# Performance work log

Hardware: AMD Instinct MI355X
Metric: run time of the kernel (lower is better)

Reference implementation:

```python
import jax, jax.numpy as jnp
import numpy as np

N = 4096       # num nodes
E = 131072     # num edges (avg degree 32)
IN = 128       # in_channels
H = 256        # hidden_channels
NC = 16        # num_classes
NH = 4         # num_heads
HD = H // NH   # head dim
EPS = 1e-5


def setup_inputs() -> dict:
    key = jax.random.key(0)
    ks = jax.random.split(key, 16)
    p = lambda k, sh, s=0.05: jax.random.normal(k, sh, jnp.float32) * s
    return {
        "x": jax.random.normal(ks[0], (N, IN), jnp.float32),
        "edge_index": jax.random.randint(ks[1], (2, E), 0, N),
        "edge_attr": jax.random.uniform(ks[2], (E,), jnp.float32),
        # GCN layers
        "W_gcn1": p(ks[3], (IN, H)), "b_gcn1": jnp.zeros((H,), jnp.float32),
        "W_gcn2": p(ks[4], (H, H)), "b_gcn2": jnp.zeros((H,), jnp.float32),
        # Transformer encoder layer (post-norm, batch_first)
        "in_proj_w": p(ks[5], (3 * H, H)), "in_proj_b": jnp.zeros((3 * H,), jnp.float32),
        "out_proj_w": p(ks[6], (H, H)), "out_proj_b": jnp.zeros((H,), jnp.float32),
        "ln1_g": jnp.ones((H,), jnp.float32), "ln1_b": jnp.zeros((H,), jnp.float32),
        "ffn_w1": p(ks[7], (H, 4 * H)), "ffn_b1": jnp.zeros((4 * H,), jnp.float32),
        "ffn_w2": p(ks[8], (4 * H, H)), "ffn_b2": jnp.zeros((H,), jnp.float32),
        "ln2_g": jnp.ones((H,), jnp.float32), "ln2_b": jnp.zeros((H,), jnp.float32),
        # classifier head
        "W_cls": p(ks[9], (H, NC)), "b_cls": jnp.zeros((NC,), jnp.float32),
        # semantic decoder
        "W_d1": p(ks[10], (H, 2 * H)), "b_d1": jnp.zeros((2 * H,), jnp.float32),
        "W_d2": p(ks[11], (2 * H, 3)), "b_d2": jnp.zeros((3,), jnp.float32),
    }


def gcn_conv(x, edge_index, edge_weight, W, b):
    """PyG GCNConv: add self-loops, symmetric norm, gather-matmul-scatter."""
    n = x.shape[0]
    src, dst = edge_index[0], edge_index[1]
    loop = jnp.arange(n)
    src_f = jnp.concatenate([src, loop])
    dst_f = jnp.concatenate([dst, loop])
    ew_f = jnp.concatenate([edge_weight, jnp.ones((n,), x.dtype)])
    deg = jax.ops.segment_sum(ew_f, dst_f, num_segments=n)
    dinv = jnp.where(deg > 0, jax.lax.rsqrt(deg), 0.0)
    norm = dinv[src_f] * ew_f * dinv[dst_f]            # [E+N]
    h = x @ W                                          # [N,H]
    out = jax.ops.segment_sum(norm[:, None] * h[src_f], dst_f, num_segments=n)
    return out + b


def layer_norm(x, g, b):
    mu = jnp.mean(x, axis=-1, keepdims=True)
    var = jnp.mean(jnp.square(x - mu), axis=-1, keepdims=True)
    return (x - mu) * jax.lax.rsqrt(var + EPS) * g + b


def transformer_layer(x, in_proj_w, in_proj_b, out_proj_w, out_proj_b,
                      ln1_g, ln1_b, ffn_w1, ffn_b1, ffn_w2, ffn_b2, ln2_g, ln2_b):
    # Self-attention (seq = all N nodes, batch of 1), eval mode (no dropout)
    qkv = x @ in_proj_w.T + in_proj_b                  # [N,3H]
    q, k, v = jnp.split(qkv, 3, axis=-1)
    q = q.reshape(-1, NH, HD) * (1.0 / np.sqrt(HD))
    k = k.reshape(-1, NH, HD)
    v = v.reshape(-1, NH, HD)
    scores = jnp.einsum("nhd,mhd->hnm", q, k)          # [NH,N,N]
    attn = jax.nn.softmax(scores, axis=-1)
    ctx = jnp.einsum("hnm,mhd->nhd", attn, v).reshape(-1, H)
    attn_out = ctx @ out_proj_w.T + out_proj_b
    x = layer_norm(x + attn_out, ln1_g, ln1_b)         # post-norm
    ffn = jax.nn.relu(x @ ffn_w1 + ffn_b1) @ ffn_w2 + ffn_b2
    return layer_norm(x + ffn, ln2_g, ln2_b)


def reference(x, edge_index, edge_attr,
              W_gcn1, b_gcn1, W_gcn2, b_gcn2,
              in_proj_w, in_proj_b, out_proj_w, out_proj_b,
              ln1_g, ln1_b, ffn_w1, ffn_b1, ffn_w2, ffn_b2, ln2_g, ln2_b,
              W_cls, b_cls, W_d1, b_d1, W_d2, b_d2):
    x_local = jax.nn.relu(gcn_conv(x, edge_index, edge_attr, W_gcn1, b_gcn1))
    # F.dropout with training=False is identity
    x_local = gcn_conv(x_local, edge_index, edge_attr, W_gcn2, b_gcn2)
    x_global = transformer_layer(x_local, in_proj_w, in_proj_b, out_proj_w,
                                 out_proj_b, ln1_g, ln1_b, ffn_w1, ffn_b1,
                                 ffn_w2, ffn_b2, ln2_g, ln2_b)
    x_final = x_local + x_global
    out_cls = jax.nn.log_softmax(x_final @ W_cls + b_cls, axis=1)
    out_reco = jax.nn.sigmoid(jax.nn.relu(x_final @ W_d1 + b_d1) @ W_d2 + b_d2)
    return (out_cls, out_reco)
```

## Files before the change

### kernel.cpp

```cpp
#include <hip/hip_runtime.h>
#include <hip/hip_bf16.h>

#define N_NODES 4096
#define N_EDGES 131072
#define KSPLIT 4

typedef short bf16x8 __attribute__((ext_vector_type(8)));
typedef float f32x4  __attribute__((ext_vector_type(4)));

static __device__ __forceinline__ float b2f(__hip_bfloat16 x) { return __bfloat162float(x); }
static __device__ __forceinline__ __hip_bfloat16 f2b(float x) { return __float2bfloat16(x); }
static __device__ __forceinline__ short f2bs(float x) {
    __hip_bfloat16 h = __float2bfloat16(x);
    return *reinterpret_cast<short*>(&h);
}
static __device__ __forceinline__ float us2f(ushort u) {
    union { unsigned i; float f; } x; x.i = ((unsigned)u) << 16; return x.f;
}

static __device__ __forceinline__ float rmax16(float v) {
    v = fmaxf(v, __shfl_xor(v, 1));
    v = fmaxf(v, __shfl_xor(v, 2));
    v = fmaxf(v, __shfl_xor(v, 4));
    v = fmaxf(v, __shfl_xor(v, 8));
    return v;
}
static __device__ __forceinline__ float rsum16(float v) {
    v += __shfl_xor(v, 1);
    v += __shfl_xor(v, 2);
    v += __shfl_xor(v, 4);
    v += __shfl_xor(v, 8);
    return v;
}

__global__ void probe_k(const unsigned* __restrict__ ln1g_raw,
                        const unsigned* __restrict__ ei_raw, int* flags) {
    if (threadIdx.x == 0 && blockIdx.x == 0) {
        flags[0] = (ln1g_raw[0] == 0x3F800000u) ? 1 : 0;
        unsigned acc = 0;
        for (int j = 1; j < 32; j += 2) acc |= ei_raw[j];
        flags[1] = (acc == 0u) ? 1 : 0;
    }
}

struct Ptrs24 { const void* p[24]; };

#define CAST_TOTAL 1681171

__global__ __launch_bounds__(256) void cast_all(Ptrs24 ptrs, const int* __restrict__ flags,
                                                __hip_bfloat16* __restrict__ canon) {
    const int sizes[24] = {524288,131072,32768,256,65536,256,196608,768,65536,256,
                           256,256,262144,1024,262144,256,256,256,4096,16,
                           131072,512,1536,3};
    int i = blockIdx.x * 256 + threadIdx.x;
    if (i >= CAST_TOTAL) return;
    const int f32 = flags[0];
    int off = i, seg = 0, base = 0;
    bool done = false;
#pragma unroll
    for (int s = 0; s < 24; s++) {
        if (!done) {
            if (off < sizes[s]) { seg = s; done = true; }
            else { off -= sizes[s]; base += sizes[s]; }
        }
    }
    float v = f32 ? ((const float*)ptrs.p[seg])[off]
                  : b2f(((const __hip_bfloat16*)ptrs.p[seg])[off]);
    int dst = off;
    if (seg == 2)       dst = (off & 255)  * 128  + (off >> 8);
    else if (seg == 4)  dst = (off & 255)  * 256  + (off >> 8);
    else if (seg == 12) dst = (off & 1023) * 256  + (off >> 10);
    else if (seg == 14) dst = (off & 255)  * 1024 + (off >> 8);
    else if (seg == 20) dst = (off & 511)  * 256  + (off >> 9);
    canon[base + dst] = f2b(v);
}

static __device__ __forceinline__ int ld_idx(const void* ei, int k, int i64) {
    return i64 ? (int)((const long long*)ei)[k] : ((const int*)ei)[k];
}

__global__ __launch_bounds__(256) void deg_init_k(float* deg, int* cnt) {
    int i = blockIdx.x * 256 + threadIdx.x;
    if (i < N_NODES) { deg[i] = 1.0f; cnt[i] = 0; }
}

__global__ __launch_bounds__(256) void deg_scat_k(const void* __restrict__ ei,
                                                  const __hip_bfloat16* __restrict__ ew,
                                                  const int* __restrict__ flags,
                                                  float* deg, int* cnt) {
    int e = blockIdx.x * 256 + threadIdx.x;
    if (e < N_EDGES) {
        int d = ld_idx(ei, N_EDGES + e, flags[1]);
        atomicAdd(&deg[d], b2f(ew[e]));
        atomicAdd(&cnt[d], 1);
    }
}

__global__ __launch_bounds__(256) void scan_k(const float* __restrict__ deg, float* dinv,
                                              int* cnt, int* rowptr) {
    __shared__ int ss[256];
    const int t = threadIdx.x;
    const int base = t * 16;
    int loc[16];
    int run = 0;
#pragma unroll
    for (int j = 0; j < 16; j++) { loc[j] = run; run += cnt[base + j]; }
    ss[t] = run;
    __syncthreads();
    for (int off = 1; off < 256; off <<= 1) {
        int v = (t >= off) ? ss[t - off] : 0;
        __syncthreads();
        ss[t] += v;
        __syncthreads();
    }
    int pre = (t == 0) ? 0 : ss[t - 1];
#pragma unroll
    for (int j = 0; j < 16; j++) rowptr[base + j] = pre + loc[j];
    if (t == 255) rowptr[N_NODES] = pre + run;
    for (int i = t; i < N_NODES; i += 256) {
        float dg = deg[i];
        dinv[i] = dg > 0.f ? rsqrtf(dg) : 0.f;
        cnt[i] = 0;
    }
}

__global__ __launch_bounds__(256) void fill_k(const void* __restrict__ ei,
                                              const __hip_bfloat16* __restrict__ ew,
                                              const int* __restrict__ flags,
                                              const float* __restrict__ dinv,
                                              const int* __restrict__ rowptr,
                                              int* cur, int* csrc, float* cw) {
    int e = blockIdx.x * 256 + threadIdx.x;
    if (e < N_EDGES) {
        int i64 = flags[1];
        int s = ld_idx(ei, e, i64), d = ld_idx(ei, N_EDGES + e, i64);
        int p = atomicAdd(&cur[d], 1);
        int slot = rowptr[d] + p;
        csrc[slot] = s;
        cw[slot] = dinv[s] * b2f(ew[e]) * dinv[d];
    }
}

template <bool RELU>
__global__ __launch_bounds__(256) void gcn_agg(const __hip_bfloat16* __restrict__ hf,
                                               const float* __restrict__ dinv,
                                               const int* __restrict__ rowptr,
                                               const int* __restrict__ csrc,
                                               const float* __restrict__ cw,
                                               const __hip_bfloat16* __restrict__ bias,
                                               __hip_bfloat16* __restrict__ out) {
    const int t = threadIdx.x;
    const int n = blockIdx.x * 4 + (t >> 6);
    const int c0 = (t & 63) * 4;
    const ushort* hp = (const ushort*)hf;
    const float di = dinv[n];
    float acc[4];
    {
        ushort4 own = *(const ushort4*)(hp + (size_t)n * 256 + c0);
        ushort4 bv  = *(const ushort4*)((const ushort*)bias + c0);
        const float dii = di * di;
        acc[0] = fmaf(dii, us2f(own.x), us2f(bv.x));
        acc[1] = fmaf(dii, us2f(own.y), us2f(bv.y));
        acc[2] = fmaf(dii, us2f(own.z), us2f(bv.z));
        acc[3] = fmaf(dii, us2f(own.w), us2f(bv.w));
    }
    int p = rowptr[n];
    const int end = rowptr[n + 1];
    for (; p + 4 <= end; p += 4) {
        int s0 = csrc[p], s1 = csrc[p + 1], s2 = csrc[p + 2], s3 = csrc[p + 3];
        float w0 = cw[p], w1 = cw[p + 1], w2 = cw[p + 2], w3 = cw[p + 3];
        ushort4 v0 = *(const ushort4*)(hp + (size_t)s0 * 256 + c0);
        ushort4 v1 = *(const ushort4*)(hp + (size_t)s1 * 256 + c0);
        ushort4 v2 = *(const ushort4*)(hp + (size_t)s2 * 256 + c0);
        ushort4 v3 = *(const ushort4*)(hp + (size_t)s3 * 256 + c0);
        acc[0] = fmaf(w0, us2f(v0.x), acc[0]); acc[1] = fmaf(w0, us2f(v0.y), acc[1]);
        acc[2] = fmaf(w0, us2f(v0.z), acc[2]); acc[3] = fmaf(w0, us2f(v0.w), acc[3]);
        acc[0] = fmaf(w1, us2f(v1.x), acc[0]); acc[1] = fmaf(w1, us2f(v1.y), acc[1]);
        acc[2] = fmaf(w1, us2f(v1.z), acc[2]); acc[3] = fmaf(w1, us2f(v1.w), acc[3]);
        acc[0] = fmaf(w2, us2f(v2.x), acc[0]); acc[1] = fmaf(w2, us2f(v2.y), acc[1]);
        acc[2] = fmaf(w2, us2f(v2.z), acc[2]); acc[3] = fmaf(w2, us2f(v2.w), acc[3]);
        acc[0] = fmaf(w3, us2f(v3.x), acc[0]); acc[1] = fmaf(w3, us2f(v3.y), acc[1]);
        acc[2] = fmaf(w3, us2f(v3.z), acc[2]); acc[3] = fmaf(w3, us2f(v3.w), acc[3]);
    }
    for (; p < end; p++) {
        int s = csrc[p];
        float wgt = cw[p];
        ushort4 v = *(const ushort4*)(hp + (size_t)s * 256 + c0);
        acc[0] = fmaf(wgt, us2f(v.x), acc[0]); acc[1] = fmaf(wgt, us2f(v.y), acc[1]);
        acc[2] = fmaf(wgt, us2f(v.z), acc[2]); acc[3] = fmaf(wgt, us2f(v.w), acc[3]);
    }
    if (RELU) {
#pragma unroll
        for (int j = 0; j < 4; j++) acc[j] = fmaxf(acc[j], 0.f);
    }
    ushort4 o;
    o.x = (ushort)f2bs(acc[0]); o.y = (ushort)f2bs(acc[1]);
    o.z = (ushort)f2bs(acc[2]); o.w = (ushort)f2bs(acc[3]);
    *(ushort4*)((ushort*)out + (size_t)n * 256 + c0) = o;
}

template <bool BIAS, bool RELU>
__global__ __launch_bounds__(256) void gemm64(const __hip_bfloat16* __restrict__ A,
                                              const __hip_bfloat16* __restrict__ Bt,
                                              const __hip_bfloat16* __restrict__ bias,
                                              __hip_bfloat16* __restrict__ C,
                                              int K, int Nn) {
    __shared__ __align__(16) short As[64 * 40];
    __shared__ __align__(16) short Bs[64 * 40];
    const int t = threadIdx.x;
    const int m0 = blockIdx.y * 64, n0 = blockIdx.x * 64;
    const int lane = t & 63, w = t >> 6, li = lane & 15, g = lane >> 4;

    f32x4 acc[4];
#pragma unroll
    for (int i = 0; i < 4; i++) acc[i] = (f32x4){0.f, 0.f, 0.f, 0.f};

    const int arow = (t * 8) >> 5;
    const int acol = (t * 8) & 31;

    for (int k0 = 0; k0 < K; k0 += 32) {
        {
            uint4 v = *(const uint4*)((const ushort*)A + (size_t)(m0 + arow) * K + k0 + acol);
            *(uint4*)&As[arow * 40 + acol] = v;
            uint4 b = *(const uint4*)((const ushort*)Bt + (size_t)(n0 + arow) * K + k0 + acol);
            *(uint4*)&Bs[arow * 40 + acol] = b;
        }
        __syncthreads();
        bf16x8 a = *(const bf16x8*)&As[(w * 16 + li) * 40 + g * 8];
#pragma unroll
        for (int nt = 0; nt < 4; nt++) {
            bf16x8 b = *(const bf16x8*)&Bs[(nt * 16 + li) * 40 + g * 8];
            acc[nt] = __builtin_amdgcn_mfma_f32_16x16x32_bf16(a, b, acc[nt], 0, 0, 0);
        }
        __syncthreads();
    }
#pragma unroll
    for (int nt = 0; nt < 4; nt++) {
        const int col = n0 + nt * 16 + li;
        const float bv = BIAS ? b2f(bias[col]) : 0.f;
#pragma unroll
        for (int r = 0; r < 4; r++) {
            const int row = m0 + w * 16 + g * 4 + r;
            float v = acc[nt][r] + bv;
            if (RELU) v = fmaxf(v, 0.f);
            C[(size_t)row * Nn + col] = f2b(v);
        }
    }
}

__global__ __launch_bounds__(256) void attn_part(const __hip_bfloat16* __restrict__ qkv,
                                                 float* __restrict__ Opart,
                                                 float2* __restrict__ MLpart) {
    __shared__ __align__(16) short Qs[64 * 72];
    __shared__ __align__(16) short Ks[64 * 72];
    __shared__ __align__(16) short Vt[64 * 72];
    __shared__ __align__(16) short Ps[64 * 72];
    const int t = threadIdx.x;
    const int h = blockIdx.y;
    const int q0 = blockIdx.x * 64;
    const int kz = blockIdx.z;
    const int lane = t & 63, w = t >> 6, li = lane & 15, g = lane >> 4;

#pragma unroll
    for (int it = 0; it < 2; it++) {
        int idx = it * 256 + t;
        int r = idx >> 3, d = (idx & 7) * 8;
        uint4 v = *(const uint4*)((const ushort*)qkv + (size_t)(q0 + r) * 768 + h * 64 + d);
        *(uint4*)&Qs[r * 72 + d] = v;
    }

    f32x4 O[4];
#pragma unroll
    for (int i = 0; i < 4; i++) O[i] = (f32x4){0.f, 0.f, 0.f, 0.f};
    float m_run[4], l_run[4];
#pragma unroll
    for (int r = 0; r < 4; r++) { m_run[r] = -1e30f; l_run[r] = 0.f; }

    const int jbeg = kz * 1024;
    for (int j0 = jbeg; j0 < jbeg + 1024; j0 += 64) {
#pragma unroll
        for (int it = 0; it < 2; it++) {
            int idx = it * 256 + t;
            int r = idx >> 3, d = (idx & 7) * 8;
            uint4 kv = *(const uint4*)((const ushort*)qkv + (size_t)(j0 + r) * 768 + 256 + h * 64 + d);
            *(uint4*)&Ks[r * 72 + d] = kv;
        }
#pragma unroll
        for (int it = 0; it < 2; it++) {
            int dblk = it * 4 + w;
            uint4 vv = *(const uint4*)((const ushort*)qkv + (size_t)(j0 + lane) * 768 + 512 + h * 64 + dblk * 8);
            const short* sv = (const short*)&vv;
#pragma unroll
            for (int j = 0; j < 8; j++) Vt[(dblk * 8 + j) * 72 + lane] = sv[j];
        }
        __syncthreads();

        f32x4 S[4];
#pragma unroll
        for (int i = 0; i < 4; i++) S[i] = (f32x4){0.f, 0.f, 0.f, 0.f};
#pragma unroll
        for (int kk = 0; kk < 64; kk += 32) {
            bf16x8 a = *(const bf16x8*)&Qs[(w * 16 + li) * 72 + kk + g * 8];
#pragma unroll
            for (int nt = 0; nt < 4; nt++) {
                bf16x8 b = *(const bf16x8*)&Ks[(nt * 16 + li) * 72 + kk + g * 8];
                S[nt] = __builtin_amdgcn_mfma_f32_16x16x32_bf16(a, b, S[nt], 0, 0, 0);
            }
        }

        float alpha[4];
#pragma unroll
        for (int r = 0; r < 4; r++) {
            float mx = -1e30f;
#pragma unroll
            for (int nt = 0; nt < 4; nt++) {
                S[nt][r] *= 0.125f;
                mx = fmaxf(mx, S[nt][r]);
            }
            mx = rmax16(mx);
            float mnew = fmaxf(m_run[r], mx);
            alpha[r] = __expf(m_run[r] - mnew);
            m_run[r] = mnew;
            float rs = 0.f;
#pragma unroll
            for (int nt = 0; nt < 4; nt++) {
                float p = __expf(S[nt][r] - mnew);
                S[nt][r] = p;
                rs += p;
            }
            rs = rsum16(rs);
            l_run[r] = l_run[r] * alpha[r] + rs;
        }
#pragma unroll
        for (int nt = 0; nt < 4; nt++)
#pragma unroll
            for (int r = 0; r < 4; r++) {
                Ps[(w * 16 + g * 4 + r) * 72 + nt * 16 + li] = f2bs(S[nt][r]);
                O[nt][r] *= alpha[r];
            }
        __syncthreads();

#pragma unroll
        for (int kk = 0; kk < 64; kk += 32) {
            bf16x8 a = *(const bf16x8*)&Ps[(w * 16 + li) * 72 + kk + g * 8];
#pragma unroll
            for (int nt = 0; nt < 4; nt++) {
                bf16x8 b = *(const bf16x8*)&Vt[(nt * 16 + li) * 72 + kk + g * 8];
                O[nt] = __builtin_amdgcn_mfma_f32_16x16x32_bf16(a, b, O[nt], 0, 0, 0);
            }
        }
        __syncthreads();
    }

    const int hb = kz * 4 + h;
#pragma unroll
    for (int nt = 0; nt < 4; nt++)
#pragma unroll
        for (int r = 0; r < 4; r++) {
            int lr = w * 16 + g * 4 + r;
            Opart[((size_t)hb * 4096 + q0 + lr) * 64 + nt * 16 + li] = O[nt][r];
        }
    if (li == 0) {
#pragma unroll
        for (int r = 0; r < 4; r++) {
            int lr = w * 16 + g * 4 + r;
            MLpart[(size_t)hb * 4096 + q0 + lr] = make_float2(m_run[r], l_run[r]);
        }
    }
}

__global__ __launch_bounds__(256) void attn_comb(const float* __restrict__ Opart,
                                                 const float2* __restrict__ MLpart,
                                                 __hip_bfloat16* __restrict__ ctx) {
    const int t = threadIdx.x;
    const int h = blockIdx.y;
    const int row = blockIdx.x * 64 + (t >> 2);
    const int d0 = (t & 3) * 16;
    float m[KSPLIT], l[KSPLIT];
    float M = -1e30f;
#pragma unroll
    for (int s = 0; s < KSPLIT; s++) {
        float2 ml = MLpart[(size_t)(s * 4 + h) * 4096 + row];
        m[s] = ml.x; l[s] = ml.y;
        M = fmaxf(M, m[s]);
    }
    float L = 0.f, wgt[KSPLIT];
#pragma unroll
    for (int s = 0; s < KSPLIT; s++) { wgt[s] = __expf(m[s] - M); L += l[s] * wgt[s]; }
    const float inv = 1.f / L;
    float o[16];
#pragma unroll
    for (int j = 0; j < 16; j++) o[j] = 0.f;
#pragma unroll
    for (int s = 0; s < KSPLIT; s++) {
        const float* base = Opart + ((size_t)(s * 4 + h) * 4096 + row) * 64 + d0;
#pragma unroll
        for (int q = 0; q < 4; q++) {
            f32x4 v = *(const f32x4*)(base + q * 4);
#pragma unroll
            for (int j = 0; j < 4; j++) o[q * 4 + j] = fmaf(wgt[s], v[j], o[q * 4 + j]);
        }
    }
    ushort pk[16];
#pragma unroll
    for (int j = 0; j < 16; j++) pk[j] = (ushort)f2bs(o[j] * inv);
    ushort* dst = (ushort*)ctx + (size_t)row * 256 + h * 64 + d0;
    *(uint4*)dst = *(uint4*)pk;
    *(uint4*)(dst + 8) = *(uint4*)(pk + 8);
}

template <bool ADDC>
__global__ __launch_bounds__(256) void ln256(const __hip_bfloat16* __restrict__ A,
                                             const __hip_bfloat16* __restrict__ Bv,
                                             const __hip_bfloat16* __restrict__ gw,
                                             const __hip_bfloat16* __restrict__ bw,
                                             const __hip_bfloat16* __restrict__ Cadd,
                                             __hip_bfloat16* __restrict__ out) {
    __shared__ float red[8];
    const int row = blockIdx.x, c = threadIdx.x;
    const size_t o = (size_t)row * 256 + c;
    float x = b2f(A[o]) + b2f(Bv[o]);
    float s = x;
#pragma unroll
    for (int m = 1; m < 64; m <<= 1) s += __shfl_xor(s, m);
    const int wv = c >> 6;
    if ((c & 63) == 0) red[wv] = s;
    __syncthreads();
    float mu = (red[0] + red[1] + red[2] + red[3]) * (1.f / 256.f);
    float d = x - mu;
    float s2 = d * d;
#pragma unroll
    for (int m = 1; m < 64; m <<= 1) s2 += __shfl_xor(s2, m);
    if ((c & 63) == 0) red[4 + wv] = s2;
    __syncthreads();
    float var = (red[4] + red[5] + red[6] + red[7]) * (1.f / 256.f);
    float y = d * rsqrtf(var + 1e-5f) * b2f(gw[c]) + b2f(bw[c]);
    if (ADDC) y += b2f(Cadd[o]);
    out[o] = f2b(y);
}

__global__ __launch_bounds__(256) void cls16(const __hip_bfloat16* __restrict__ xf,
                                             const __hip_bfloat16* __restrict__ W,
                                             const __hip_bfloat16* __restrict__ b,
                                             const int* __restrict__ flags,
                                             void* __restrict__ out) {
    __shared__ float Ws[256 * 16];
    __shared__ float bs[16];
    const int t = threadIdx.x;
    for (int i = t; i < 4096; i += 256) Ws[i] = b2f(W[i]);
    if (t < 16) bs[t] = b2f(b[t]);
    __syncthreads();
    const int c = t & 15, rl = t >> 4;
    const int row = blockIdx.x * 16 + rl;
    const ushort* xr = (const ushort*)xf + (size_t)row * 256;
    float acc = bs[c];
    for (int k0 = 0; k0 < 256; k0 += 8) {
        uint4 v = *(const uint4*)(xr + k0);
        const ushort* sv = (const ushort*)&v;
#pragma unroll
        for (int j = 0; j < 8; j++) acc = fmaf(us2f(sv[j]), Ws[(k0 + j) * 16 + c], acc);
    }
    float mx = rmax16(acc);
    float se = rsum16(__expf(acc - mx));
    float v = acc - mx - __logf(se);
    const size_t oidx = (size_t)row * 16 + c;
    if (flags[0]) ((float*)out)[oidx] = v;
    else          ((__hip_bfloat16*)out)[oidx] = f2b(v);
}

__global__ __launch_bounds__(256) void reco3(const __hip_bfloat16* __restrict__ hid,
                                             const __hip_bfloat16* __restrict__ W,
                                             const __hip_bfloat16* __restrict__ b,
                                             const int* __restrict__ flags,
                                             void* __restrict__ out) {
    __shared__ float Ws[512 * 3];
    const int t = threadIdx.x;
    for (int i = t; i < 1536; i += 256) Ws[i] = b2f(W[i]);
    __syncthreads();
    const int c = t & 3, rl = t >> 2;
    const int row = blockIdx.x * 64 + rl;
    if (c < 3) {
        float acc = b2f(b[c]);
        const ushort* hr = (const ushort*)hid + (size_t)row * 512;
        for (int k0 = 0; k0 < 512; k0 += 8) {
            uint4 v = *(const uint4*)(hr + k0);
            const ushort* sv = (const ushort*)&v;
#pragma unroll
            for (int j = 0; j < 8; j++) acc = fmaf(us2f(sv[j]), Ws[(k0 + j) * 3 + c], acc);
        }
        float v = 1.f / (1.f + __expf(-acc));
        const size_t oidx = (size_t)(N_NODES * 16) + (size_t)row * 3 + c;
        if (flags[0]) ((float*)out)[oidx] = v;
        else          ((__hip_bfloat16*)out)[oidx] = f2b(v);
    }
}

extern "C" void kernel_launch(void* const* d_in, const int* in_sizes, int n_in,
                              void* d_out, int out_size, void* d_ws, size_t ws_size,
                              hipStream_t stream) {
    char* ws = (char*)d_ws;
    int*   flags  = (int*)(ws + 0);
    __hip_bfloat16* canon = (__hip_bfloat16*)(ws + 256);
    float* deg    = (float*)(ws + 3362816);
    int*   cnt    = (int*)  (ws + 3379200);
    int*   rowptr = (int*)  (ws + 3395584);
    float* dinv   = (float*)(ws + 3412224);
    int*   csrc   = (int*)  (ws + 3428608);
    float* cw     = (float*)(ws + 3952896);
    __hip_bfloat16* h     = (__hip_bfloat16*)(ws + 4477184);
    __hip_bfloat16* x1    = (__hip_bfloat16*)(ws + 6574336);
    __hip_bfloat16* xloc  = (__hip_bfloat16*)(ws + 8671488);
    __hip_bfloat16* big   = (__hip_bfloat16*)(ws + 10768640);
    __hip_bfloat16* ctxp  = (__hip_bfloat16*)(ws + 19157248);
    __hip_bfloat16* attno = (__hip_bfloat16*)(ws + 21254400);
    __hip_bfloat16* y1    = (__hip_bfloat16*)(ws + 23351552);
    __hip_bfloat16* xfin  = (__hip_bfloat16*)(ws + 25448704);
    float*  Opart  = (float*) (ws + 27545856);
    float2* MLpart = (float2*)(ws + 44323072);

    const __hip_bfloat16* xc    = canon + 0;
    const __hip_bfloat16* eac   = canon + 524288;
    const __hip_bfloat16* Wg1   = canon + 655360;
    const __hip_bfloat16* bg1   = canon + 688128;
    const __hip_bfloat16* Wg2   = canon + 688384;
    const __hip_bfloat16* bg2   = canon + 753920;
    const __hip_bfloat16* ipw   = canon + 754176;
    const __hip_bfloat16* ipb   = canon + 950784;
    const __hip_bfloat16* opw   = canon + 951552;
    const __hip_bfloat16* opb   = canon + 1017088;
    const __hip_bfloat16* ln1g  = canon + 1017344;
    const __hip_bfloat16* ln1b  = canon + 1017600;
    const __hip_bfloat16* fw1   = canon + 1017856;
    const __hip_bfloat16* fb1   = canon + 1280000;
    const __hip_bfloat16* fw2   = canon + 1281024;
    const __hip_bfloat16* fb2   = canon + 1543168;
    const __hip_bfloat16* ln2g  = canon + 1543424;
    const __hip_bfloat16* ln2b  = canon + 1543680;
    const __hip_bfloat16* Wcls  = canon + 1543936;
    const __hip_bfloat16* bcls  = canon + 1548032;
    const __hip_bfloat16* Wd1   = canon + 1548048;
    const __hip_bfloat16* bd1   = canon + 1679120;
    const __hip_bfloat16* Wd2   = canon + 1679632;
    const __hip_bfloat16* bd2   = canon + 1681168;

    const void* ei = d_in[1];

    Ptrs24 pt;
    {
        const int map[24] = {0,2,3,4,5,6,7,8,9,10,11,12,13,14,15,16,17,18,19,20,21,22,23,24};
        for (int i = 0; i < 24; i++) pt.p[i] = d_in[map[i]];
    }

    const dim3 b256(256);

    probe_k<<<1, 64, 0, stream>>>((const unsigned*)d_in[11], (const unsigned*)d_in[1], flags);
    cast_all<<<(CAST_TOTAL + 255) / 256, b256, 0, stream>>>(pt, flags, canon);

    deg_init_k<<<16, b256, 0, stream>>>(deg, cnt);
    deg_scat_k<<<512, b256, 0, stream>>>(ei, eac, flags, deg, cnt);
    scan_k<<<1, b256, 0, stream>>>(deg, dinv, cnt, rowptr);
    fill_k<<<512, b256, 0, stream>>>(ei, eac, flags, dinv, rowptr, cnt, csrc, cw);

    gemm64<false, false><<<dim3(4, 64), b256, 0, stream>>>(xc, Wg1, nullptr, h, 128, 256);
    gcn_agg<true><<<1024, b256, 0, stream>>>(h, dinv, rowptr, csrc, cw, bg1, x1);
    gemm64<false, false><<<dim3(4, 64), b256, 0, stream>>>(x1, Wg2, nullptr, h, 256, 256);
    gcn_agg<false><<<1024, b256, 0, stream>>>(h, dinv, rowptr, csrc, cw, bg2, xloc);

    gemm64<true, false><<<dim3(12, 64), b256, 0, stream>>>(xloc, ipw, ipb, big, 256, 768);
    attn_part<<<dim3(64, 4, KSPLIT), b256, 0, stream>>>(big, Opart, MLpart);
    attn_comb<<<dim3(64, 4), b256, 0, stream>>>(Opart, MLpart, ctxp);
    gemm64<true, false><<<dim3(4, 64), b256, 0, stream>>>(ctxp, opw, opb, attno, 256, 256);
    ln256<false><<<4096, b256, 0, stream>>>(xloc, attno, ln1g, ln1b, nullptr, y1);
    gemm64<true, true><<<dim3(16, 64), b256, 0, stream>>>(y1, fw1, fb1, big, 256, 1024);
    gemm64<true, false><<<dim3(4, 64), b256, 0, stream>>>(big, fw2, fb2, ctxp, 1024, 256);
    ln256<true><<<4096, b256, 0, stream>>>(y1, ctxp, ln2g, ln2b, xloc, xfin);

    cls16<<<256, b256, 0, stream>>>(xfin, Wcls, bcls, flags, d_out);
    gemm64<true, true><<<dim3(8, 64), b256, 0, stream>>>(xfin, Wd1, bd1, big, 256, 512);
    reco3<<<64, b256, 0, stream>>>(big, Wd2, bd2, flags, d_out);
}
```

Measured before the change: 330.4 us.

## Transpose attention scores to keep P in registers, double KSPLIT, bf16 partials

The attention kernel now computes S^T with swapped MFMA operands and moves P into the PV MFMA A-operand layout with lane shuffles. This removes the Ps shared-memory round trip and one barrier per tile. KSPLIT grows from 4 to 8 for more parallelism, and the split partial outputs are stored in bf16 instead of fp32 to halve combine traffic. The GEMM tile depth doubles to K=64 per barrier pair. Risks include lower precision in the partials and MLpart now aliasing the x1 buffer region, which is only safe if x1 is dead by then.

```diff
diff --git a/kernel.cpp b/kernel.cpp
--- a/kernel.cpp
+++ b/kernel.cpp
@@ -3,7 +3,7 @@
 
 #define N_NODES 4096
 #define N_EDGES 131072
-#define KSPLIT 4
+#define KSPLIT 8
 
 typedef short bf16x8 __attribute__((ext_vector_type(8)));
 typedef float f32x4  __attribute__((ext_vector_type(4)));
@@ -16,6 +16,9 @@
 }
 static __device__ __forceinline__ float us2f(ushort u) {
     union { unsigned i; float f; } x; x.i = ((unsigned)u) << 16; return x.f;
+}
+static __device__ __forceinline__ unsigned pack2(float lo, float hi) {
+    return (unsigned)(ushort)f2bs(lo) | ((unsigned)(ushort)f2bs(hi) << 16);
 }
 
 static __device__ __forceinline__ float rmax16(float v) {
@@ -205,32 +208,35 @@
                                               const __hip_bfloat16* __restrict__ bias,
                                               __hip_bfloat16* __restrict__ C,
                                               int K, int Nn) {
-    __shared__ __align__(16) short As[64 * 40];
-    __shared__ __align__(16) short Bs[64 * 40];
+    __shared__ __align__(16) short As[64 * 72];
+    __shared__ __align__(16) short Bs[64 * 72];
     const int t = threadIdx.x;
     const int m0 = blockIdx.y * 64, n0 = blockIdx.x * 64;
-    const int lane = t & 63, w = t >> 6, li = lane & 15, g = lane >> 4;
+    const int lane = t & 63, w = t >> 6, li = lane & 15, quad = lane >> 4;
 
     f32x4 acc[4];
 #pragma unroll
     for (int i = 0; i < 4; i++) acc[i] = (f32x4){0.f, 0.f, 0.f, 0.f};
 
-    const int arow = (t * 8) >> 5;
-    const int acol = (t * 8) & 31;
-
-    for (int k0 = 0; k0 < K; k0 += 32) {
-        {
-            uint4 v = *(const uint4*)((const ushort*)A + (size_t)(m0 + arow) * K + k0 + acol);
-            *(uint4*)&As[arow * 40 + acol] = v;
-            uint4 b = *(const uint4*)((const ushort*)Bt + (size_t)(n0 + arow) * K + k0 + acol);
-            *(uint4*)&Bs[arow * 40 + acol] = b;
+    for (int k0 = 0; k0 < K; k0 += 64) {
+#pragma unroll
+        for (int i = 0; i < 2; i++) {
+            int idx = i * 256 + t;
+            int r = idx >> 3, c8 = (idx & 7) * 8;
+            uint4 va = *(const uint4*)((const ushort*)A + (size_t)(m0 + r) * K + k0 + c8);
+            *(uint4*)&As[r * 72 + c8] = va;
+            uint4 vb = *(const uint4*)((const ushort*)Bt + (size_t)(n0 + r) * K + k0 + c8);
+            *(uint4*)&Bs[r * 72 + c8] = vb;
         }
         __syncthreads();
-        bf16x8 a = *(const bf16x8*)&As[(w * 16 + li) * 40 + g * 8];
-#pragma unroll
-        for (int nt = 0; nt < 4; nt++) {
-            bf16x8 b = *(const bf16x8*)&Bs[(nt * 16 + li) * 40 + g * 8];
-            acc[nt] = __builtin_amdgcn_mfma_f32_16x16x32_bf16(a, b, acc[nt], 0, 0, 0);
+#pragma unroll
+        for (int kk = 0; kk < 64; kk += 32) {
+            bf16x8 a = *(const bf16x8*)&As[(w * 16 + li) * 72 + kk + quad * 8];
+#pragma unroll
+            for (int nt = 0; nt < 4; nt++) {
+                bf16x8 b = *(const bf16x8*)&Bs[(nt * 16 + li) * 72 + kk + quad * 8];
+                acc[nt] = __builtin_amdgcn_mfma_f32_16x16x32_bf16(a, b, acc[nt], 0, 0, 0);
+            }
         }
         __syncthreads();
     }
@@ -240,7 +246,7 @@
         const float bv = BIAS ? b2f(bias[col]) : 0.f;
 #pragma unroll
         for (int r = 0; r < 4; r++) {
-            const int row = m0 + w * 16 + g * 4 + r;
+            const int row = m0 + w * 16 + quad * 4 + r;
             float v = acc[nt][r] + bv;
             if (RELU) v = fmaxf(v, 0.f);
             C[(size_t)row * Nn + col] = f2b(v);
@@ -249,17 +255,16 @@
 }
 
 __global__ __launch_bounds__(256) void attn_part(const __hip_bfloat16* __restrict__ qkv,
-                                                 float* __restrict__ Opart,
+                                                 __hip_bfloat16* __restrict__ Opart,
                                                  float2* __restrict__ MLpart) {
     __shared__ __align__(16) short Qs[64 * 72];
     __shared__ __align__(16) short Ks[64 * 72];
     __shared__ __align__(16) short Vt[64 * 72];
-    __shared__ __align__(16) short Ps[64 * 72];
     const int t = threadIdx.x;
     const int h = blockIdx.y;
     const int q0 = blockIdx.x * 64;
     const int kz = blockIdx.z;
-    const int lane = t & 63, w = t >> 6, li = lane & 15, g = lane >> 4;
+    const int lane = t & 63, w = t >> 6, li = lane & 15, quad = lane >> 4;
 
 #pragma unroll
     for (int it = 0; it < 2; it++) {
@@ -272,12 +277,14 @@
     f32x4 O[4];
 #pragma unroll
     for (int i = 0; i < 4; i++) O[i] = (f32x4){0.f, 0.f, 0.f, 0.f};
-    float m_run[4], l_run[4];
-#pragma unroll
-    for (int r = 0; r < 4; r++) { m_run[r] = -1e30f; l_run[r] = 0.f; }
-
-    const int jbeg = kz * 1024;
-    for (int j0 = jbeg; j0 < jbeg + 1024; j0 += 64) {
+    float m_run = -1e30f, l_run = 0.f;
+
+    const int srcA = 32 * (quad & 1) + li;
+    const int srcB = srcA + 16;
+    const int hi_t = (quad >> 1) & 1;
+
+    const int jbeg = kz * (N_NODES / KSPLIT);
+    for (int j0 = jbeg; j0 < jbeg + N_NODES / KSPLIT; j0 += 64) {
 #pragma unroll
         for (int it = 0; it < 2; it++) {
             int idx = it * 256 + t;
@@ -295,81 +302,98 @@
         }
         __syncthreads();
 
-        f32x4 S[4];
-#pragma unroll
-        for (int i = 0; i < 4; i++) S[i] = (f32x4){0.f, 0.f, 0.f, 0.f};
+        f32x4 T[4];
+#pragma unroll
+        for (int i = 0; i < 4; i++) T[i] = (f32x4){0.f, 0.f, 0.f, 0.f};
 #pragma unroll
         for (int kk = 0; kk < 64; kk += 32) {
-            bf16x8 a = *(const bf16x8*)&Qs[(w * 16 + li) * 72 + kk + g * 8];
+            bf16x8 qf = *(const bf16x8*)&Qs[(w * 16 + li) * 72 + kk + quad * 8];
 #pragma unroll
             for (int nt = 0; nt < 4; nt++) {
-                bf16x8 b = *(const bf16x8*)&Ks[(nt * 16 + li) * 72 + kk + g * 8];
-                S[nt] = __builtin_amdgcn_mfma_f32_16x16x32_bf16(a, b, S[nt], 0, 0, 0);
+                bf16x8 kf = *(const bf16x8*)&Ks[(nt * 16 + li) * 72 + kk + quad * 8];
+                T[nt] = __builtin_amdgcn_mfma_f32_16x16x32_bf16(kf, qf, T[nt], 0, 0, 0);
             }
         }
 
-        float alpha[4];
-#pragma unroll
-        for (int r = 0; r < 4; r++) {
-            float mx = -1e30f;
-#pragma unroll
-            for (int nt = 0; nt < 4; nt++) {
-                S[nt][r] *= 0.125f;
-                mx = fmaxf(mx, S[nt][r]);
+        float mx = -1e30f;
+#pragma unroll
+        for (int nt = 0; nt < 4; nt++)
+#pragma unroll
+            for (int r = 0; r < 4; r++) {
+                T[nt][r] *= 0.125f;
+                mx = fmaxf(mx, T[nt][r]);
             }
-            mx = rmax16(mx);
-            float mnew = fmaxf(m_run[r], mx);
-            alpha[r] = __expf(m_run[r] - mnew);
-            m_run[r] = mnew;
-            float rs = 0.f;
-#pragma unroll
-            for (int nt = 0; nt < 4; nt++) {
-                float p = __expf(S[nt][r] - mnew);
-                S[nt][r] = p;
+        mx = fmaxf(mx, __shfl_xor(mx, 16));
+        mx = fmaxf(mx, __shfl_xor(mx, 32));
+        float mnew = fmaxf(m_run, mx);
+        float alpha = __expf(m_run - mnew);
+        m_run = mnew;
+        float rs = 0.f;
+#pragma unroll
+        for (int nt = 0; nt < 4; nt++)
+#pragma unroll
+            for (int r = 0; r < 4; r++) {
+                float p = __expf(T[nt][r] - mnew);
+                T[nt][r] = p;
                 rs += p;
             }
-            rs = rsum16(rs);
-            l_run[r] = l_run[r] * alpha[r] + rs;
-        }
+        rs += __shfl_xor(rs, 16);
+        rs += __shfl_xor(rs, 32);
+        l_run = l_run * alpha + rs;
+
+        unsigned pd[4][2];
+#pragma unroll
+        for (int nt = 0; nt < 4; nt++) {
+            pd[nt][0] = pack2(T[nt][0], T[nt][1]);
+            pd[nt][1] = pack2(T[nt][2], T[nt][3]);
+        }
+
+        float al[4];
+#pragma unroll
+        for (int r = 0; r < 4; r++) al[r] = __shfl(alpha, quad * 4 + r);
 #pragma unroll
         for (int nt = 0; nt < 4; nt++)
 #pragma unroll
-            for (int r = 0; r < 4; r++) {
-                Ps[(w * 16 + g * 4 + r) * 72 + nt * 16 + li] = f2bs(S[nt][r]);
-                O[nt][r] *= alpha[r];
+            for (int r = 0; r < 4; r++) O[nt][r] *= al[r];
+
+#pragma unroll
+        for (int c = 0; c < 2; c++) {
+            const int tl = 2 * c, th = 2 * c + 1;
+            unsigned aL0 = (unsigned)__shfl((int)pd[tl][0], srcA);
+            unsigned aL1 = (unsigned)__shfl((int)pd[tl][1], srcA);
+            unsigned aH0 = (unsigned)__shfl((int)pd[th][0], srcA);
+            unsigned aH1 = (unsigned)__shfl((int)pd[th][1], srcA);
+            unsigned bL0 = (unsigned)__shfl((int)pd[tl][0], srcB);
+            unsigned bL1 = (unsigned)__shfl((int)pd[tl][1], srcB);
+            unsigned bH0 = (unsigned)__shfl((int)pd[th][0], srcB);
+            unsigned bH1 = (unsigned)__shfl((int)pd[th][1], srcB);
+            unsigned af[4];
+            af[0] = hi_t ? aH0 : aL0;
+            af[1] = hi_t ? aH1 : aL1;
+            af[2] = hi_t ? bH0 : bL0;
+            af[3] = hi_t ? bH1 : bL1;
+            bf16x8 afrag = *(const bf16x8*)af;
+#pragma unroll
+            for (int nt2 = 0; nt2 < 4; nt2++) {
+                bf16x8 vf = *(const bf16x8*)&Vt[(nt2 * 16 + li) * 72 + c * 32 + quad * 8];
+                O[nt2] = __builtin_amdgcn_mfma_f32_16x16x32_bf16(afrag, vf, O[nt2], 0, 0, 0);
             }
+        }
         __syncthreads();
-
-#pragma unroll
-        for (int kk = 0; kk < 64; kk += 32) {
-            bf16x8 a = *(const bf16x8*)&Ps[(w * 16 + li) * 72 + kk + g * 8];
-#pragma unroll
-            for (int nt = 0; nt < 4; nt++) {
-                bf16x8 b = *(const bf16x8*)&Vt[(nt * 16 + li) * 72 + kk + g * 8];
-                O[nt] = __builtin_amdgcn_mfma_f32_16x16x32_bf16(a, b, O[nt], 0, 0, 0);
-            }
-        }
-        __syncthreads();
     }
 
     const int hb = kz * 4 + h;
+    ushort* ob = (ushort*)Opart + ((size_t)hb * 4096 + q0) * 64;
 #pragma unroll
     for (int nt = 0; nt < 4; nt++)
 #pragma unroll
-        for (int r = 0; r < 4; r++) {
-            int lr = w * 16 + g * 4 + r;
-            Opart[((size_t)hb * 4096 + q0 + lr) * 64 + nt * 16 + li] = O[nt][r];
-        }
-    if (li == 0) {
-#pragma unroll
-        for (int r = 0; r < 4; r++) {
-            int lr = w * 16 + g * 4 + r;
-            MLpart[(size_t)hb * 4096 + q0 + lr] = make_float2(m_run[r], l_run[r]);
-        }
-    }
-}
-
-__global__ __launch_bounds__(256) void attn_comb(const float* __restrict__ Opart,
+        for (int r = 0; r < 4; r++)
+            ob[(size_t)(w * 16 + quad * 4 + r) * 64 + nt * 16 + li] = (ushort)f2bs(O[nt][r]);
+    if (quad == 0)
+        MLpart[(size_t)hb * 4096 + q0 + w * 16 + li] = make_float2(m_run, l_run);
+}
+
+__global__ __launch_bounds__(256) void attn_comb(const __hip_bfloat16* __restrict__ Opart,
                                                  const float2* __restrict__ MLpart,
                                                  __hip_bfloat16* __restrict__ ctx) {
     const int t = threadIdx.x;
@@ -393,12 +417,15 @@
     for (int j = 0; j < 16; j++) o[j] = 0.f;
 #pragma unroll
     for (int s = 0; s < KSPLIT; s++) {
-        const float* base = Opart + ((size_t)(s * 4 + h) * 4096 + row) * 64 + d0;
-#pragma unroll
-        for (int q = 0; q < 4; q++) {
-            f32x4 v = *(const f32x4*)(base + q * 4);
-#pragma unroll
-            for (int j = 0; j < 4; j++) o[q * 4 + j] = fmaf(wgt[s], v[j], o[q * 4 + j]);
+        const ushort* base = (const ushort*)Opart + ((size_t)(s * 4 + h) * 4096 + row) * 64 + d0;
+        uint4 v0 = *(const uint4*)base;
+        uint4 v1 = *(const uint4*)(base + 8);
+        const ushort* sv0 = (const ushort*)&v0;
+        const ushort* sv1 = (const ushort*)&v1;
+#pragma unroll
+        for (int j = 0; j < 8; j++) {
+            o[j]     = fmaf(wgt[s], us2f(sv0[j]), o[j]);
+            o[8 + j] = fmaf(wgt[s], us2f(sv1[j]), o[8 + j]);
         }
     }
     ushort pk[16];
@@ -515,8 +542,8 @@
     __hip_bfloat16* attno = (__hip_bfloat16*)(ws + 21254400);
     __hip_bfloat16* y1    = (__hip_bfloat16*)(ws + 23351552);
     __hip_bfloat16* xfin  = (__hip_bfloat16*)(ws + 25448704);
-    float*  Opart  = (float*) (ws + 27545856);
-    float2* MLpart = (float2*)(ws + 44323072);
+    __hip_bfloat16* Opart = (__hip_bfloat16*)(ws + 27545856);
+    float2* MLpart = (float2*)(ws + 6574336);
 
     const __hip_bfloat16* xc    = canon + 0;
     const __hip_bfloat16* eac   = canon + 524288;
```

Result: no change. 332.8 us (+0.7%).
